# Kernel optimization log

Hardware: AMD Instinct MI355X
Metric: run time of the kernel (lower is better)

The kernel has to match this reference:

```python
import jax, jax.numpy as jnp
import numpy as np
import math

VOCAB = 128
READ_DIM = 128
LOGIT_SCALE = 1.0 / 16.0
NUM_FF = 6
CARRY_DIM = 896
D_MODEL = CARRY_DIM + READ_DIM


def ste_sign(x):
    # forward of the STE sign: +-1, zero -> +1
    return jnp.where(x >= 0, 1.0, -1.0).astype(x.dtype)


def ste_round(x):
    return jnp.round(x)


def setup_inputs() -> dict:
    key = jax.random.key(0)
    k_tok, k_init, k_emb, k_ff, k_head, k_thr = jax.random.split(key, 6)
    tokens = jax.random.randint(k_tok, (64, 512), 0, VOCAB, dtype=jnp.int64) if jax.config.read('jax_enable_x64') else jax.random.randint(k_tok, (64, 512), 0, VOCAB, dtype=jnp.int32)
    initial_lat = jax.random.uniform(k_init, (D_MODEL,), minval=-1.0, maxval=1.0)
    embed_lat = jax.random.uniform(k_emb, (VOCAB, READ_DIM), minval=-1.0, maxval=1.0)
    ff_lat = jax.random.uniform(k_ff, (NUM_FF, D_MODEL, D_MODEL), minval=-1.0, maxval=1.0)
    head_lat = jax.random.uniform(k_head, (READ_DIM, VOCAB), minval=-1.0, maxval=1.0)
    ff_thresh_lat = jax.random.uniform(k_thr, (NUM_FF, D_MODEL), minval=-2.0, maxval=2.0)
    return {
        'tokens': tokens,
        'initial_lat': initial_lat,
        'embed_lat': embed_lat,
        'ff_lat': ff_lat,
        'head_lat': head_lat,
        'ff_thresh_lat': ff_thresh_lat,
    }


def reference(tokens, initial_lat, embed_lat, ff_lat, head_lat, ff_thresh_lat):
    B, T = tokens.shape
    num_ff = ff_lat.shape[0]
    d_model = initial_lat.shape[0]
    carry_dim = d_model - READ_DIM
    act_scale = math.sqrt(d_model)

    initial = ste_sign(initial_lat)          # [d_model]
    embed = ste_sign(embed_lat)              # [VOCAB, read_dim]
    ff = ste_sign(ff_lat)                    # [num_ff, d_model, d_model]
    head = ste_sign(head_lat)                # [read_dim, VOCAB]
    thr = ste_round(ff_thresh_lat)           # [num_ff, d_model]

    x0 = jnp.broadcast_to(initial[None, :], (B, d_model))

    def step(x, tok_t):
        # tok_t: [B]
        h = x
        for i in range(num_ff):
            pre = h @ ff[i]                  # [B, d_model]
            h = ste_sign((pre - thr[i]) / act_scale)
        carry = h[:, :carry_dim]
        read = h[:, carry_dim:]
        logits = read @ head * LOGIT_SCALE   # [B, VOCAB]
        logp = jax.nn.log_softmax(logits, axis=-1)
        loss_t = -jnp.mean(jnp.take_along_axis(logp, tok_t[:, None], axis=1))
        x_new = jnp.concatenate([carry, embed[tok_t]], axis=1)
        return x_new, loss_t

    _, losses = jax.lax.scan(step, x0, tokens.T)  # scan over T
    return jnp.mean(losses)
```

## Files before the change

### kernel.cpp

```cpp
#include <hip/hip_runtime.h>
#include <stdint.h>

typedef unsigned long long u64;

#define VOCAB 128
#define RD 128
#define DM 1024
#define NFF 6
#define BATCH 64
#define TSTEPS 512


__global__ void pack_ff(const float* __restrict__ ff, u64* __restrict__ ffb) {
    int wid  = blockIdx.x * (blockDim.x >> 6) + (threadIdx.x >> 6);
    int lane = threadIdx.x & 63;
    int jt = wid & 15;
    int w  = (wid >> 4) & 15;
    int i  = wid >> 8;
    int j  = jt * 64 + lane;
    const float* src = ff + ((size_t)(i * DM) + w * 64) * DM + j;
    u64 word = 0;
#pragma unroll
    for (int b = 0; b < 64; ++b) {
        float v = src[(size_t)b * DM];
        word |= (u64)(v < 0.0f) << b;
    }
    ffb[((i * 16 + w) << 10) + j] = word;
}

__global__ void pack_small(const float* __restrict__ emb, const float* __restrict__ head,
                           u64* __restrict__ eb, u64* __restrict__ hb) {
    int tid = threadIdx.x;
    if (tid < 128) {
        int v = tid;
        for (int wd = 0; wd < 2; ++wd) {
            u64 word = 0;
            for (int l = 0; l < 64; ++l)
                word |= (u64)(emb[v * RD + wd * 64 + l] < 0.0f) << l;
            eb[v * 2 + wd] = word;
        }
    } else {
        int v = tid - 128;
        for (int wd = 0; wd < 2; ++wd) {
            u64 word = 0;
            for (int l = 0; l < 64; ++l)
                word |= (u64)(head[(wd * 64 + l) * VOCAB + v] < 0.0f) << l;
            hb[v * 2 + wd] = word;
        }
    }
}

__global__ void __launch_bounds__(1024, 4)
brnn_main(const int* __restrict__ tokens,
          const float* __restrict__ initial_lat,
          const float* __restrict__ thr_lat,
          const u64* __restrict__ ffb,
          const u64* __restrict__ eb,
          const u64* __restrict__ hb,
          double* __restrict__ losses) {
    const int b    = blockIdx.x;
    const int tid  = threadIdx.x;
    const int lane = tid & 63;
    const int wv   = tid >> 6;

    __shared__ __align__(16) u64 hbuf[2][16];

    u64 fr[NFF][16];
#pragma unroll
    for (int i = 0; i < NFF; ++i)
#pragma unroll
        for (int w = 0; w < 16; ++w) {
            u64 v = ffb[((i * 16 + w) << 10) + tid];
            asm volatile("" : "+a"(v));
            fr[i][w] = v;
        }

    int cthr[NFF];
#pragma unroll
    for (int i = 0; i < NFF; ++i) {
        int thr = (int)rintf(thr_lat[i * DM + tid]);
        cthr[i] = ((DM - thr) >> 1) + 1;
    }

    u64 h0a = hb[lane * 2 + 0];
    u64 h0b = hb[lane * 2 + 1];
    u64 h1a = hb[(lane + 64) * 2 + 0];
    u64 h1b = hb[(lane + 64) * 2 + 1];
    asm volatile("" : "+a"(h0a), "+a"(h0b), "+a"(h1a), "+a"(h1b));

    {
        u64 m = __ballot(initial_lat[tid] < 0.0f);
        if (lane == 0) hbuf[0][wv] = m;
    }
    __syncthreads();

    const int* toks = tokens + b * TSTEPS;
    double lacc = 0.0;
    int p = 0;

    for (int t = 0; t < TSTEPS; ++t) {
        int tok = toks[t];

        u64 enew = 0;
        if (wv == 0 && lane < 2) enew = eb[tok * 2 + lane];

#pragma unroll
        for (int i = 0; i < NFF; ++i) {
            const ulonglong2* hp = (const ulonglong2*)hbuf[p];
            int acc = 0;
#pragma unroll
            for (int q = 0; q < 8; ++q) {
                ulonglong2 hv = hp[q];
                acc += __popcll(hv.x ^ fr[i][2 * q]) + __popcll(hv.y ^ fr[i][2 * q + 1]);
            }
            u64 m = __ballot(acc >= cthr[i]);
            if (lane == 0) hbuf[p ^ 1][wv] = m;
            p ^= 1;
            __syncthreads();
        }

        if (wv == 0) {
            u64 r0 = hbuf[p][14], r1 = hbuf[p][15];
            int d0 = 128 - 2 * (__popcll(r0 ^ h0a) + __popcll(r1 ^ h0b));
            int d1 = 128 - 2 * (__popcll(r0 ^ h1a) + __popcll(r1 ^ h1b));
            float l0 = (float)d0 * (1.0f / 16.0f);
            float l1 = (float)d1 * (1.0f / 16.0f);
            float mx = fmaxf(l0, l1);
#pragma unroll
            for (int s = 32; s >= 1; s >>= 1) mx = fmaxf(mx, __shfl_xor(mx, s));
            float se = __expf(l0 - mx) + __expf(l1 - mx);
#pragma unroll
            for (int s = 32; s >= 1; s >>= 1) se += __shfl_xor(se, s);
            int   tl   = tok & 63;
            float la   = __shfl(l0, tl);
            float lb   = __shfl(l1, tl);
            float ltok = (tok >> 6) ? lb : la;
            lacc += (double)(mx + __logf(se) - ltok);
            if (lane < 2) hbuf[p][14 + lane] = enew;
        }
        __syncthreads();
    }

    if (tid == 0) losses[b] = lacc;
}

__global__ void reduce_loss(const double* __restrict__ losses, float* __restrict__ out) {
    int lane = threadIdx.x;
    double v = losses[lane];
#pragma unroll
    for (int s = 32; s >= 1; s >>= 1) v += __shfl_down(v, s);
    if (lane == 0) out[0] = (float)(v * (1.0 / ((double)BATCH * (double)TSTEPS)));
}

extern "C" void kernel_launch(void* const* d_in, const int* in_sizes, int n_in,
                              void* d_out, int out_size, void* d_ws, size_t ws_size,
                              hipStream_t stream) {
    const int*   tokens  = (const int*)d_in[0];
    const float* initial = (const float*)d_in[1];
    const float* embed   = (const float*)d_in[2];
    const float* ff      = (const float*)d_in[3];
    const float* head    = (const float*)d_in[4];
    const float* thrl    = (const float*)d_in[5];

    char* ws = (char*)d_ws;
    u64*    ffb    = (u64*)ws;
    u64*    eb     = (u64*)(ws + 786432);
    u64*    hb     = (u64*)(ws + 786432 + 2048);
    double* losses = (double*)(ws + 786432 + 4096);

    pack_ff<<<384, 256, 0, stream>>>(ff, ffb);
    pack_small<<<1, 256, 0, stream>>>(embed, head, eb, hb);
    brnn_main<<<BATCH, 1024, 0, stream>>>(tokens, initial, thrl, ffb, eb, hb, losses);
    reduce_loss<<<1, 64, 0, stream>>>(losses, (float*)d_out);
}
```

Baseline: 7.047 ms.

## Stream transposed FF weights from cache with one-layer-ahead prefetch instead of registers

Previously each thread kept all six layers of packed binary weights resident in registers. Now the packed weights are stored transposed so each thread's 16 words for a layer are contiguous, and each layer's weights are loaded from global memory (expected to hit L2) one layer ahead of use. The goal is to free most of the register file. In exchange every time step re-reads about 768 KB per block from cache, with latency only partly hidden behind the short per-layer compute. The head weights move to LDS, and __syncthreads is replaced by a raw s_barrier with only an LDS waitcnt.

```diff
diff --git a/kernel.cpp b/kernel.cpp
--- a/kernel.cpp
+++ b/kernel.cpp
@@ -11,7 +11,13 @@
 #define TSTEPS 512
 
 
-__global__ void pack_ff(const float* __restrict__ ff, u64* __restrict__ ffb) {
+#define BARRIER()                                            \
+    do {                                                     \
+        asm volatile("s_waitcnt lgkmcnt(0)" ::: "memory");   \
+        __builtin_amdgcn_s_barrier();                        \
+    } while (0)
+
+__global__ void pack_ff(const float* __restrict__ ff, u64* __restrict__ ffbT) {
     int wid  = blockIdx.x * (blockDim.x >> 6) + (threadIdx.x >> 6);
     int lane = threadIdx.x & 63;
     int jt = wid & 15;
@@ -25,7 +31,7 @@
         float v = src[(size_t)b * DM];
         word |= (u64)(v < 0.0f) << b;
     }
-    ffb[((i * 16 + w) << 10) + j] = word;
+    ffbT[((size_t)((i << 10) + j)) * 16 + w] = word;
 }
 
 __global__ void pack_small(const float* __restrict__ emb, const float* __restrict__ head,
@@ -54,7 +60,7 @@
 brnn_main(const int* __restrict__ tokens,
           const float* __restrict__ initial_lat,
           const float* __restrict__ thr_lat,
-          const u64* __restrict__ ffb,
+          const u64* __restrict__ ffbT,
           const u64* __restrict__ eb,
           const u64* __restrict__ hb,
           double* __restrict__ losses) {
@@ -64,16 +70,9 @@
     const int wv   = tid >> 6;
 
     __shared__ __align__(16) u64 hbuf[2][16];
+    __shared__ u64 hbL[2 * VOCAB];
 
-    u64 fr[NFF][16];
-#pragma unroll
-    for (int i = 0; i < NFF; ++i)
-#pragma unroll
-        for (int w = 0; w < 16; ++w) {
-            u64 v = ffb[((i * 16 + w) << 10) + tid];
-            asm volatile("" : "+a"(v));
-            fr[i][w] = v;
-        }
+    if (tid < 2 * VOCAB) hbL[tid] = hb[tid];
 
     int cthr[NFF];
 #pragma unroll
@@ -82,45 +81,64 @@
         cthr[i] = ((DM - thr) >> 1) + 1;
     }
 
-    u64 h0a = hb[lane * 2 + 0];
-    u64 h0b = hb[lane * 2 + 1];
-    u64 h1a = hb[(lane + 64) * 2 + 0];
-    u64 h1b = hb[(lane + 64) * 2 + 1];
-    asm volatile("" : "+a"(h0a), "+a"(h0b), "+a"(h1a), "+a"(h1b));
+    u64 c[16];
+    {
+        const ulonglong2* wp = (const ulonglong2*)(ffbT + (size_t)tid * 16);
+#pragma unroll
+        for (int k = 0; k < 8; ++k) {
+            ulonglong2 v = wp[k];
+            c[2 * k] = v.x; c[2 * k + 1] = v.y;
+        }
+    }
 
     {
         u64 m = __ballot(initial_lat[tid] < 0.0f);
         if (lane == 0) hbuf[0][wv] = m;
     }
-    __syncthreads();
+    BARRIER();
 
     const int* toks = tokens + b * TSTEPS;
     double lacc = 0.0;
-    int p = 0;
+    int tok = toks[0];
 
     for (int t = 0; t < TSTEPS; ++t) {
-        int tok = toks[t];
+        int tok_next = toks[(t + 1 < TSTEPS) ? (t + 1) : (TSTEPS - 1)];
 
         u64 enew = 0;
         if (wv == 0 && lane < 2) enew = eb[tok * 2 + lane];
 
+        int p = 0;
 #pragma unroll
         for (int i = 0; i < NFF; ++i) {
+            const int nl = (i + 1) % NFF;
+            const ulonglong2* wp =
+                (const ulonglong2*)(ffbT + ((size_t)(nl << 10) + tid) * 16);
+            ulonglong2 n0 = wp[0], n1 = wp[1], n2 = wp[2], n3 = wp[3],
+                       n4 = wp[4], n5 = wp[5], n6 = wp[6], n7 = wp[7];
+
             const ulonglong2* hp = (const ulonglong2*)hbuf[p];
             int acc = 0;
 #pragma unroll
             for (int q = 0; q < 8; ++q) {
                 ulonglong2 hv = hp[q];
-                acc += __popcll(hv.x ^ fr[i][2 * q]) + __popcll(hv.y ^ fr[i][2 * q + 1]);
+                acc += __popcll(hv.x ^ c[2 * q]) + __popcll(hv.y ^ c[2 * q + 1]);
             }
             u64 m = __ballot(acc >= cthr[i]);
             if (lane == 0) hbuf[p ^ 1][wv] = m;
+
+            c[0] = n0.x;  c[1] = n0.y;  c[2] = n1.x;  c[3] = n1.y;
+            c[4] = n2.x;  c[5] = n2.y;  c[6] = n3.x;  c[7] = n3.y;
+            c[8] = n4.x;  c[9] = n4.y;  c[10] = n5.x; c[11] = n5.y;
+            c[12] = n6.x; c[13] = n6.y; c[14] = n7.x; c[15] = n7.y;
+
+            BARRIER();
             p ^= 1;
-            __syncthreads();
         }
 
         if (wv == 0) {
-            u64 r0 = hbuf[p][14], r1 = hbuf[p][15];
+            u64 r0 = hbuf[0][14], r1 = hbuf[0][15];
+            u64 h0a = hbL[lane * 2 + 0],        h0b = hbL[lane * 2 + 1];
+            u64 h1a = hbL[(lane + 64) * 2 + 0], h1b = hbL[(lane + 64) * 2 + 1];
             int d0 = 128 - 2 * (__popcll(r0 ^ h0a) + __popcll(r1 ^ h0b));
             int d1 = 128 - 2 * (__popcll(r0 ^ h1a) + __popcll(r1 ^ h1b));
             float l0 = (float)d0 * (1.0f / 16.0f);
@@ -136,9 +154,10 @@
             float lb   = __shfl(l1, tl);
             float ltok = (tok >> 6) ? lb : la;
             lacc += (double)(mx + __logf(se) - ltok);
-            if (lane < 2) hbuf[p][14 + lane] = enew;
+            if (lane < 2) hbuf[0][14 + lane] = enew;
         }
-        __syncthreads();
+        BARRIER();
+        tok = tok_next;
     }
 
     if (tid == 0) losses[b] = lacc;
@@ -163,13 +182,13 @@
     const float* thrl    = (const float*)d_in[5];
 
     char* ws = (char*)d_ws;
-    u64*    ffb    = (u64*)ws;
+    u64*    ffbT   = (u64*)ws;
     u64*    eb     = (u64*)(ws + 786432);
     u64*    hb     = (u64*)(ws + 786432 + 2048);
     double* losses = (double*)(ws + 786432 + 4096);
 
-    pack_ff<<<384, 256, 0, stream>>>(ff, ffb);
+    pack_ff<<<384, 256, 0, stream>>>(ff, ffbT);
     pack_small<<<1, 256, 0, stream>>>(embed, head, eb, hb);
-    brnn_main<<<BATCH, 1024, 0, stream>>>(tokens, initial, thrl, ffb, eb, hb, losses);
+    brnn_main<<<BATCH, 1024, 0, stream>>>(tokens, initial, thrl, ffbT, eb, hb, losses);
     reduce_loss<<<1, 64, 0, stream>>>(losses, (float*)d_out);
 }
```

After: 10.05 ms. 42.6% more time.
